# Optimization experiments

Hardware: AMD Instinct MI355X
Metric: run time of the kernel (lower is better)

The kernel has to match this reference:

```python
import jax, jax.numpy as jnp
import numpy as np

B, T, INPUT = 8, 16, 64
OUTPUT = 128
N_IN, N_TR, N_ACT = 32, 192, 32
N = N_IN + N_TR + N_ACT
H = 256   # neuron_hidden_dim
KQ = 256  # key_query_dim
S = 256   # signal_dim

def _xavier(key, shape):
    fan_in, fan_out = shape[-2], shape[-1]
    lim = np.sqrt(6.0 / (fan_in + fan_out)).astype(np.float32)
    return jax.random.uniform(key, shape, jnp.float32, -lim, lim)

def setup_inputs() -> dict:
    key = jax.random.key(0)
    ks = jax.random.split(key, 10)
    return {
        'x': jax.random.normal(ks[0], (B, T, INPUT), jnp.float32),
        'w_rec_input': _xavier(ks[1], (N_IN, INPUT, H)),
        'b_rec_input': jnp.zeros((N_IN, H), jnp.float32),
        'w_rec_other': _xavier(ks[2], (N_TR + N_ACT, S, H)),
        'b_rec_other': jnp.zeros((N_TR + N_ACT, H), jnp.float32),
        'w_lstm_ih': _xavier(ks[3], (N, H, 4 * H)),
        'b_lstm_ih': jnp.zeros((N, 4 * H), jnp.float32),
        'w_lstm_hh': _xavier(ks[4], (N, H, 4 * H)),
        'b_lstm_hh': jnp.zeros((N, 4 * H), jnp.float32),
        'w_query': _xavier(ks[5], (N, H, KQ)),
        'b_query': jnp.zeros((N, KQ), jnp.float32),
        'w_key': _xavier(ks[6], (N, H, KQ)),
        'b_key': jnp.zeros((N, KQ), jnp.float32),
        'w_sender': _xavier(ks[7], (N, H, S)),
        'b_sender': jnp.zeros((N, S), jnp.float32),
        'w_proj': _xavier(ks[8], (OUTPUT, N_ACT * S)),  # nn.Linear weight [out, in]
        'b_proj': jnp.zeros((OUTPUT,), jnp.float32),
    }

def reference(x, w_rec_input, b_rec_input, w_rec_other, b_rec_other,
              w_lstm_ih, b_lstm_ih, w_lstm_hh, b_lstm_hh,
              w_query, b_query, w_key, b_key, w_sender, b_sender,
              w_proj, b_proj):
    batch = x.shape[0]
    scale = 1.0 / np.sqrt(KQ).astype(np.float32)

    def step(carry, x_t):
        h, c, prev = carry  # [B,N,H], [B,N,H], [B,N,S]
        Q = jnp.einsum('bnh,nhk->bnk', h, w_query) + b_query
        K = jnp.einsum('bnh,nhk->bnk', h, w_key) + b_key
        scores = jnp.einsum('bnk,bmk->bnm', Q, K) * scale
        weights = jax.nn.softmax(scores, axis=2)
        ctx = jnp.einsum('bnm,bms->bns', weights, prev)  # [B,N,S]
        rec_in = jnp.einsum('bi,nih->bnh', x_t, w_rec_input) + b_rec_input  # [B,N_IN,H]
        rec_oth = jnp.einsum('bns,nsh->bnh', ctx[:, N_IN:, :], w_rec_other) + b_rec_other
        lstm_in = jax.nn.relu(jnp.concatenate([rec_in, rec_oth], axis=1))  # [B,N,H]
        gates = (jnp.einsum('bnh,nhg->bng', lstm_in, w_lstm_ih) + b_lstm_ih
                 + jnp.einsum('bnh,nhg->bng', h, w_lstm_hh) + b_lstm_hh)
        i_g, f_g, g_g, o_g = jnp.split(gates, 4, axis=2)
        c_new = jax.nn.sigmoid(f_g) * c + jax.nn.sigmoid(i_g) * jnp.tanh(g_g)
        h_new = jax.nn.sigmoid(o_g) * jnp.tanh(c_new)
        prev_new = jnp.einsum('bnh,nhs->bns', h_new, w_sender) + b_sender
        action = prev_new[:, -N_ACT:, :].reshape(batch, -1)
        out = action @ w_proj.T + b_proj
        return (h_new, c_new, prev_new), out

    init = (jnp.zeros((batch, N, H), x.dtype),
            jnp.zeros((batch, N, H), x.dtype),
            jnp.zeros((batch, N, S), x.dtype))
    _, outs = jax.lax.scan(step, init, jnp.swapaxes(x, 0, 1))  # outs: [T,B,OUTPUT]
    return jnp.swapaxes(outs, 0, 1)
```

## Files before the change

kernel.cpp:

```cpp
#include <hip/hip_runtime.h>
#include <cmath>

#define DEV_INLINE __device__ __forceinline__

constexpr int B_ = 8, T_ = 16, INPUT_ = 64, OUTPUT_ = 128;
constexpr int N_ = 256, H_ = 256, KQ_ = 256, S_ = 256, G_ = 1024;
constexpr int NIN_ = 32;
constexpr float SCALE_ = 0.0625f;

DEV_INLINE float sigmoid_(float x) { return 1.0f / (1.0f + expf(-x)); }
DEV_INLINE void fma4(float4& a, const float4& w, float s) {
    a.x += w.x * s; a.y += w.y * s; a.z += w.z * s; a.w += w.w * s;
}

__global__ __launch_bounds__(64)
void pnmm64_kernel(const float* __restrict__ in,
                   const float* __restrict__ W0, float* __restrict__ P0,
                   const float* __restrict__ W1, float* __restrict__ P1,
                   int n0)
{
    constexpr int KS = 4, HS = 256 / KS;
    const int ny = blockIdx.y;
    const int n = n0 + ny;
    const int split = blockIdx.x;
    const int lane = threadIdx.x;
    const int c0 = lane * 4;
    const int h0 = split * HS;
    const float* W = blockIdx.z ? W1 : W0;
    float* P = blockIdx.z ? P1 : P0;

    __shared__ float sh[HS * 8];
    for (int i = lane; i < HS * 8; i += 64) {
        int hh = i & (HS - 1), b = i >> 6;
        sh[hh * 8 + b] = in[(size_t)(b * N_ + n) * 256 + h0 + hh];
    }
    __syncthreads();

    const float* wp = W + ((size_t)ny * 256 + h0) * 256 + c0;
    float4 acc[8] = {};
    float4 bufA[8], bufB[8];
#pragma unroll
    for (int u = 0; u < 8; ++u) bufA[u] = *(const float4*)(wp + (size_t)u * 256);
#pragma unroll 1
    for (int hb = 0; hb < HS; hb += 8) {
        if (hb + 8 < HS) {
#pragma unroll
            for (int u = 0; u < 8; ++u)
                bufB[u] = *(const float4*)(wp + (size_t)(hb + 8 + u) * 256);
        }
#pragma unroll
        for (int u = 0; u < 8; ++u) {
            float4 w = bufA[u];
            const float* ip = &sh[(hb + u) * 8];
            float4 i0 = *(const float4*)ip;
            float4 i1 = *(const float4*)(ip + 4);
            fma4(acc[0], w, i0.x); fma4(acc[1], w, i0.y);
            fma4(acc[2], w, i0.z); fma4(acc[3], w, i0.w);
            fma4(acc[4], w, i1.x); fma4(acc[5], w, i1.y);
            fma4(acc[6], w, i1.z); fma4(acc[7], w, i1.w);
        }
#pragma unroll
        for (int u = 0; u < 8; ++u) bufA[u] = bufB[u];
    }
#pragma unroll
    for (int b = 0; b < 8; ++b)
        *(float4*)&P[(((size_t)split * 8 + b) * N_ + n) * 256 + c0] = acc[b];
}

__global__ __launch_bounds__(256)
void gates_mm_kernel(const float* __restrict__ lin, const float* __restrict__ hbuf,
                     const float* __restrict__ wih, const float* __restrict__ whh,
                     float* __restrict__ P)
{
    constexpr int KS = 2, HS = 256 / KS;
    const int n = blockIdx.y;
    const int split = blockIdx.x;
    const int tid = threadIdx.x;
    const int c0 = tid * 4;
    const int h0 = split * HS;

    __shared__ float shi[HS * 8];
    __shared__ float shh[HS * 8];
    for (int i = tid; i < HS * 8; i += 256) {
        int hh = i & (HS - 1), b = i >> 7;
        int src = (b * N_ + n) * H_ + h0 + hh;
        shi[hh * 8 + b] = lin[src];
        shh[hh * 8 + b] = hbuf[src];
    }
    __syncthreads();

    const float* wi = wih + ((size_t)n * H_ + h0) * G_ + c0;
    const float* wh = whh + ((size_t)n * H_ + h0) * G_ + c0;
    float4 acc[8] = {};
    float4 biA[4], bhA[4], biB[4], bhB[4];
#pragma unroll
    for (int u = 0; u < 4; ++u) {
        biA[u] = *(const float4*)(wi + (size_t)u * G_);
        bhA[u] = *(const float4*)(wh + (size_t)u * G_);
    }
#pragma unroll 1
    for (int hb = 0; hb < HS; hb += 4) {
        if (hb + 4 < HS) {
#pragma unroll
            for (int u = 0; u < 4; ++u) {
                biB[u] = *(const float4*)(wi + (size_t)(hb + 4 + u) * G_);
                bhB[u] = *(const float4*)(wh + (size_t)(hb + 4 + u) * G_);
            }
        }
#pragma unroll
        for (int u = 0; u < 4; ++u) {
            float4 a = biA[u];
            float4 h = bhA[u];
            const float* ip = &shi[(hb + u) * 8];
            const float* hp = &shh[(hb + u) * 8];
            float4 i0 = *(const float4*)ip;
            float4 i1 = *(const float4*)(ip + 4);
            float4 h0v = *(const float4*)hp;
            float4 h1v = *(const float4*)(hp + 4);
            fma4(acc[0], a, i0.x); fma4(acc[0], h, h0v.x);
            fma4(acc[1], a, i0.y); fma4(acc[1], h, h0v.y);
            fma4(acc[2], a, i0.z); fma4(acc[2], h, h0v.z);
            fma4(acc[3], a, i0.w); fma4(acc[3], h, h0v.w);
            fma4(acc[4], a, i1.x); fma4(acc[4], h, h1v.x);
            fma4(acc[5], a, i1.y); fma4(acc[5], h, h1v.y);
            fma4(acc[6], a, i1.z); fma4(acc[6], h, h1v.z);
            fma4(acc[7], a, i1.w); fma4(acc[7], h, h1v.w);
        }
#pragma unroll
        for (int u = 0; u < 4; ++u) { biA[u] = biB[u]; bhA[u] = bhB[u]; }
    }
#pragma unroll
    for (int b = 0; b < 8; ++b)
        *(float4*)&P[(((size_t)split * 8 + b) * N_ + n) * G_ + c0] = acc[b];
}

__global__ __launch_bounds__(256)
void rec_in_kernel(const float* __restrict__ x, int t,
                   const float* __restrict__ w_ri, const float* __restrict__ b_ri,
                   float* __restrict__ lin)
{
    __shared__ float sh[INPUT_ * 8];
    const int n = blockIdx.x;
    const int tid = threadIdx.x;
    for (int i = tid; i < INPUT_ * 8; i += 256) {
        int hh = i & 63, b = i >> 6;
        sh[hh * 8 + b] = x[((size_t)b * T_ + t) * INPUT_ + hh];
    }
    __syncthreads();
    const float* wp = w_ri + (size_t)n * INPUT_ * H_ + tid;
    float acc[8] = {};
#pragma unroll 8
    for (int hh = 0; hh < INPUT_; ++hh) {
        float w = wp[(size_t)hh * H_];
        float4 i0 = *(const float4*)&sh[hh * 8];
        float4 i1 = *(const float4*)&sh[hh * 8 + 4];
        acc[0] += w * i0.x; acc[1] += w * i0.y; acc[2] += w * i0.z; acc[3] += w * i0.w;
        acc[4] += w * i1.x; acc[5] += w * i1.y; acc[6] += w * i1.z; acc[7] += w * i1.w;
    }
    float bv = b_ri[n * H_ + tid];
#pragma unroll
    for (int b = 0; b < 8; ++b)
        lin[(size_t)(b * N_ + n) * H_ + tid] = fmaxf(acc[b] + bv, 0.f);
}

__global__ __launch_bounds__(256)
void reduce4_kernel(const float* __restrict__ P, const float* __restrict__ bias,
                    float* __restrict__ out, int n0, int nCount, int relu)
{
    const int idx = blockIdx.x * 256 + threadIdx.x;
    const int h4 = idx & 63;
    const int rest = idx >> 6;
    const int nn = rest % nCount;
    const int b = rest / nCount;
    const int n = n0 + nn;
    float4 s = *(const float4*)&bias[nn * 256 + h4 * 4];
#pragma unroll
    for (int sp = 0; sp < 4; ++sp) {
        float4 p = *(const float4*)&P[(((size_t)sp * 8 + b) * N_ + n) * 256 + h4 * 4];
        s.x += p.x; s.y += p.y; s.z += p.z; s.w += p.w;
    }
    if (relu) {
        s.x = fmaxf(s.x, 0.f); s.y = fmaxf(s.y, 0.f);
        s.z = fmaxf(s.z, 0.f); s.w = fmaxf(s.w, 0.f);
    }
    *(float4*)&out[((size_t)b * N_ + n) * 256 + h4 * 4] = s;
}

__global__ __launch_bounds__(256)
void reduceQK_kernel(const float* __restrict__ Pq, const float* __restrict__ Pk,
                     const float* __restrict__ bq, const float* __restrict__ bk,
                     float* __restrict__ Q, float* __restrict__ K)
{
    const int z = blockIdx.y;
    const float* P = z ? Pk : Pq;
    const float* bias = z ? bk : bq;
    float* out = z ? K : Q;
    const int idx = blockIdx.x * 256 + threadIdx.x;
    const int h4 = idx & 63;
    const int rest = idx >> 6;
    const int n = rest & 255;
    const int b = rest >> 8;
    float4 s = *(const float4*)&bias[n * 256 + h4 * 4];
#pragma unroll
    for (int sp = 0; sp < 4; ++sp) {
        float4 p = *(const float4*)&P[(((size_t)sp * 8 + b) * N_ + n) * 256 + h4 * 4];
        s.x += p.x; s.y += p.y; s.z += p.z; s.w += p.w;
    }
    *(float4*)&out[((size_t)b * N_ + n) * 256 + h4 * 4] = s;
}

__global__ void scores_kernel(const float* __restrict__ Q, const float* __restrict__ Kb,
                              float* __restrict__ sc)
{
    __shared__ float As[16][64];
    __shared__ float Bs[16][64];
    const int b = blockIdx.y;
    const int tile = blockIdx.x;
    const int row0 = (tile >> 2) * 64;
    const int col0 = (tile & 3) * 64;
    const int tid = threadIdx.x;
    const int tx = tid & 15, ty = tid >> 4;
    const int lr = tid >> 2;
    const int kq = (tid & 3) * 4;
    const float* Qb = Q + (size_t)b * N_ * KQ_;
    const float* Kbb = Kb + (size_t)b * N_ * KQ_;
    float acc[4][4] = {};
    for (int kt = 0; kt < KQ_; kt += 16) {
        float4 av = *(const float4*)&Qb[(size_t)(row0 + lr) * KQ_ + kt + kq];
        float4 bv = *(const float4*)&Kbb[(size_t)(col0 + lr) * KQ_ + kt + kq];
        __syncthreads();
        As[kq + 0][lr] = av.x; As[kq + 1][lr] = av.y; As[kq + 2][lr] = av.z; As[kq + 3][lr] = av.w;
        Bs[kq + 0][lr] = bv.x; Bs[kq + 1][lr] = bv.y; Bs[kq + 2][lr] = bv.z; Bs[kq + 3][lr] = bv.w;
        __syncthreads();
#pragma unroll
        for (int k = 0; k < 16; ++k) {
            float4 a = *(const float4*)&As[k][ty * 4];
            float4 c = *(const float4*)&Bs[k][tx * 4];
            acc[0][0] += a.x * c.x; acc[0][1] += a.x * c.y; acc[0][2] += a.x * c.z; acc[0][3] += a.x * c.w;
            acc[1][0] += a.y * c.x; acc[1][1] += a.y * c.y; acc[1][2] += a.y * c.z; acc[1][3] += a.y * c.w;
            acc[2][0] += a.z * c.x; acc[2][1] += a.z * c.y; acc[2][2] += a.z * c.z; acc[2][3] += a.z * c.w;
            acc[3][0] += a.w * c.x; acc[3][1] += a.w * c.y; acc[3][2] += a.w * c.z; acc[3][3] += a.w * c.w;
        }
    }
#pragma unroll
    for (int i = 0; i < 4; ++i) {
        float4 r = make_float4(acc[i][0] * SCALE_, acc[i][1] * SCALE_,
                               acc[i][2] * SCALE_, acc[i][3] * SCALE_);
        *(float4*)&sc[((size_t)b * N_ + row0 + ty * 4 + i) * N_ + col0 + tx * 4] = r;
    }
}

__global__ void softmax_kernel(float* __restrict__ sc)
{
    const int n = blockIdx.x, b = blockIdx.y;
    const int tid = threadIdx.x;
    __shared__ float red[256];
    float* row = sc + ((size_t)b * N_ + n) * N_;
    float v = row[tid];
    red[tid] = v;
    __syncthreads();
    for (int s = 128; s > 0; s >>= 1) {
        if (tid < s) red[tid] = fmaxf(red[tid], red[tid + s]);
        __syncthreads();
    }
    float m = red[0];
    __syncthreads();
    float e = expf(v - m);
    red[tid] = e;
    __syncthreads();
    for (int s = 128; s > 0; s >>= 1) {
        if (tid < s) red[tid] += red[tid + s];
        __syncthreads();
    }
    row[tid] = e / red[0];
}

__global__ void ctx_kernel(const float* __restrict__ W, const float* __restrict__ prev,
                           float* __restrict__ ctx)
{
    __shared__ float As[16][64];
    __shared__ float Bs[16][64];
    const int b = blockIdx.y;
    const int tile = blockIdx.x;
    const int row0 = (tile >> 2) * 64;
    const int col0 = (tile & 3) * 64;
    const int tid = threadIdx.x;
    const int tx = tid & 15, ty = tid >> 4;
    const int lr = tid >> 2;
    const int kq = (tid & 3) * 4;
    const int br = tid >> 4;
    const int bc = (tid & 15) * 4;
    const float* Wb = W + (size_t)b * N_ * N_;
    const float* pb = prev + (size_t)b * N_ * S_;
    float acc[4][4] = {};
    for (int kt = 0; kt < N_; kt += 16) {
        float4 av = *(const float4*)&Wb[(size_t)(row0 + lr) * N_ + kt + kq];
        float4 bv = *(const float4*)&pb[(size_t)(kt + br) * S_ + col0 + bc];
        __syncthreads();
        As[kq + 0][lr] = av.x; As[kq + 1][lr] = av.y; As[kq + 2][lr] = av.z; As[kq + 3][lr] = av.w;
        *(float4*)&Bs[br][bc] = bv;
        __syncthreads();
#pragma unroll
        for (int k = 0; k < 16; ++k) {
            float4 a = *(const float4*)&As[k][ty * 4];
            float4 c = *(const float4*)&Bs[k][tx * 4];
            acc[0][0] += a.x * c.x; acc[0][1] += a.x * c.y; acc[0][2] += a.x * c.z; acc[0][3] += a.x * c.w;
            acc[1][0] += a.y * c.x; acc[1][1] += a.y * c.y; acc[1][2] += a.y * c.z; acc[1][3] += a.y * c.w;
            acc[2][0] += a.z * c.x; acc[2][1] += a.z * c.y; acc[2][2] += a.z * c.z; acc[2][3] += a.z * c.w;
            acc[3][0] += a.w * c.x; acc[3][1] += a.w * c.y; acc[3][2] += a.w * c.z; acc[3][3] += a.w * c.w;
        }
    }
#pragma unroll
    for (int i = 0; i < 4; ++i) {
        float4 r = make_float4(acc[i][0], acc[i][1], acc[i][2], acc[i][3]);
        *(float4*)&ctx[((size_t)b * N_ + row0 + ty * 4 + i) * S_ + col0 + tx * 4] = r;
    }
}

__global__ __launch_bounds__(256)
void cell_kernel(const float* __restrict__ P, const float* __restrict__ bih,
                 const float* __restrict__ bhh,
                 float* __restrict__ c, float* __restrict__ h)
{
    const int tid = blockIdx.x * 256 + threadIdx.x;
    const int bn = tid >> 8;
    const int hx = tid & 255;
    const int n = bn & 255;
    const size_t PG = (size_t)8 * N_ * G_;
    const size_t gb = (size_t)bn * G_;
    float g4[4];
#pragma unroll
    for (int gi = 0; gi < 4; ++gi) {
        int off = gi * 256 + hx;
        g4[gi] = P[gb + off] + P[PG + gb + off]
               + bih[n * G_ + off] + bhh[n * G_ + off];
    }
    float cv = c[tid];
    float cn = sigmoid_(g4[1]) * cv + sigmoid_(g4[0]) * tanhf(g4[2]);
    float hn = sigmoid_(g4[3]) * tanhf(cn);
    c[tid] = cn;
    h[tid] = hn;
}

__global__ void proj_kernel(const float* __restrict__ prev, const float* __restrict__ wp,
                            const float* __restrict__ bp, float* __restrict__ out, int t)
{
    const int o = blockIdx.x;
    const int tid = threadIdx.x;
    float acc[8] = {};
    const float* wr = wp + (size_t)o * (32 * S_);
    for (int j = tid; j < 32 * S_; j += 256) {
        float w = wr[j];
#pragma unroll
        for (int b = 0; b < 8; ++b)
            acc[b] += w * prev[(size_t)b * N_ * S_ + 224 * S_ + j];
    }
    __shared__ float red[256];
#pragma unroll
    for (int b = 0; b < 8; ++b) {
        red[tid] = acc[b];
        __syncthreads();
        for (int s = 128; s > 0; s >>= 1) {
            if (tid < s) red[tid] += red[tid + s];
            __syncthreads();
        }
        if (tid == 0) out[((size_t)b * T_ + t) * OUTPUT_ + o] = red[0] + bp[o];
        __syncthreads();
    }
}

extern "C" void kernel_launch(void* const* d_in, const int* in_sizes, int n_in,
                              void* d_out, int out_size, void* d_ws, size_t ws_size,
                              hipStream_t stream)
{
    (void)in_sizes; (void)n_in; (void)out_size; (void)ws_size;
    const float* x    = (const float*)d_in[0];
    const float* w_ri = (const float*)d_in[1];
    const float* b_ri = (const float*)d_in[2];
    const float* w_ro = (const float*)d_in[3];
    const float* b_ro = (const float*)d_in[4];
    const float* w_ih = (const float*)d_in[5];
    const float* b_ih = (const float*)d_in[6];
    const float* w_hh = (const float*)d_in[7];
    const float* b_hh = (const float*)d_in[8];
    const float* w_q  = (const float*)d_in[9];
    const float* b_q  = (const float*)d_in[10];
    const float* w_k  = (const float*)d_in[11];
    const float* b_k  = (const float*)d_in[12];
    const float* w_s  = (const float*)d_in[13];
    const float* b_s  = (const float*)d_in[14];
    const float* w_p  = (const float*)d_in[15];
    const float* b_p  = (const float*)d_in[16];
    float* out = (float*)d_out;

    float* ws = (float*)d_ws;
    const size_t SZ = (size_t)B_ * N_ * H_;
    float* hbuf = ws;
    float* cbuf = hbuf + SZ;
    float* prev = cbuf + SZ;
    float* Q    = prev + SZ;
    float* Kb   = Q + SZ;
    float* sc   = Kb + SZ;
    float* ctxb = sc + SZ;
    float* lin  = ctxb + SZ;
    float* Pbuf = lin + SZ;
    float* Pq   = Pbuf;
    float* Pk   = Pbuf + 4 * SZ;
    float* Prec = Pbuf;
    float* Pg   = Pbuf;
    float* Ps   = Pbuf;

    hipMemsetAsync(d_ws, 0, 3 * SZ * sizeof(float), stream);

    for (int t = 0; t < T_; ++t) {
        pnmm64_kernel<<<dim3(4, 256, 2), 64, 0, stream>>>(hbuf, w_q, Pq, w_k, Pk, 0);
        reduceQK_kernel<<<dim3(512, 2), 256, 0, stream>>>(Pq, Pk, b_q, b_k, Q, Kb);
        scores_kernel<<<dim3(16, B_), 256, 0, stream>>>(Q, Kb, sc);
        softmax_kernel<<<dim3(N_, B_), 256, 0, stream>>>(sc);
        ctx_kernel<<<dim3(16, B_), 256, 0, stream>>>(sc, prev, ctxb);
        rec_in_kernel<<<dim3(NIN_), 256, 0, stream>>>(x, t, w_ri, b_ri, lin);
        pnmm64_kernel<<<dim3(4, 224, 1), 64, 0, stream>>>(ctxb, w_ro, Prec, w_ro, Prec, NIN_);
        reduce4_kernel<<<dim3(448), 256, 0, stream>>>(Prec, b_ro, lin, NIN_, 224, 1);
        gates_mm_kernel<<<dim3(2, 256), 256, 0, stream>>>(lin, hbuf, w_ih, w_hh, Pg);
        cell_kernel<<<dim3(2048), 256, 0, stream>>>(Pg, b_ih, b_hh, cbuf, hbuf);
        pnmm64_kernel<<<dim3(4, 256, 1), 64, 0, stream>>>(hbuf, w_s, Ps, w_s, Ps, 0);
        reduce4_kernel<<<dim3(512), 256, 0, stream>>>(Ps, b_s, prev, 0, 256, 0);
        proj_kernel<<<dim3(OUTPUT_), 256, 0, stream>>>(prev, w_p, b_p, out, t);
    }
}
```

Measured before the change: 4.483 ms.

## Fuse split-K reductions, softmax+ctx, gates+cell, and hoist input recurrence

Replaces the split-K matmul kernels plus separate reduce kernels with in-block LDS reductions that apply bias and relu directly. Merges softmax into the context matmul, gates matmul into the LSTM cell update, and computes sender/Q/K projections in one launch at the end of each step. The input-neuron recurrence is precomputed for all timesteps up front, and the projection kernel uses wave shuffles. Together these cut kernel launches and the global traffic for partial sums, at the cost of fewer, larger blocks and possibly lower occupancy.

Measured after the change: 3.922 ms. 1.14x faster.

```diff
diff --git a/kernel.cpp b/kernel.cpp
--- a/kernel.cpp
+++ b/kernel.cpp
@@ -13,37 +13,44 @@
     a.x += w.x * s; a.y += w.y * s; a.z += w.z * s; a.w += w.w * s;
 }
 
-__global__ __launch_bounds__(64)
-void pnmm64_kernel(const float* __restrict__ in,
-                   const float* __restrict__ W0, float* __restrict__ P0,
-                   const float* __restrict__ W1, float* __restrict__ P1,
-                   int n0)
-{
-    constexpr int KS = 4, HS = 256 / KS;
-    const int ny = blockIdx.y;
+__global__ __launch_bounds__(256)
+void pnmm256_kernel(const float* __restrict__ in,
+                    const float* __restrict__ W0, const float* __restrict__ bias0, float* __restrict__ O0,
+                    const float* __restrict__ W1, const float* __restrict__ bias1, float* __restrict__ O1,
+                    const float* __restrict__ W2, const float* __restrict__ bias2, float* __restrict__ O2,
+                    int n0, int nW0, int relu)
+{
+    const int ny = blockIdx.x;
     const int n = n0 + ny;
-    const int split = blockIdx.x;
-    const int lane = threadIdx.x;
+    const int nw = n - nW0;
+    const float* W; const float* bias; float* O;
+    if (blockIdx.y == 0)      { W = W0; bias = bias0; O = O0; }
+    else if (blockIdx.y == 1) { W = W1; bias = bias1; O = O1; }
+    else                      { W = W2; bias = bias2; O = O2; }
+
+    const int tid = threadIdx.x;
+    const int wv = tid >> 6;
+    const int lane = tid & 63;
     const int c0 = lane * 4;
-    const int h0 = split * HS;
-    const float* W = blockIdx.z ? W1 : W0;
-    float* P = blockIdx.z ? P1 : P0;
-
-    __shared__ float sh[HS * 8];
-    for (int i = lane; i < HS * 8; i += 64) {
-        int hh = i & (HS - 1), b = i >> 6;
-        sh[hh * 8 + b] = in[(size_t)(b * N_ + n) * 256 + h0 + hh];
-    }
-    __syncthreads();
-
-    const float* wp = W + ((size_t)ny * 256 + h0) * 256 + c0;
+    const int h0 = wv * 64;
+
+    __shared__ float sh[256 * 8];
+    __shared__ float psum[4][2048];
+
+    for (int i = tid; i < 2048; i += 256) {
+        int hh = i & 255, b = i >> 8;
+        sh[hh * 8 + b] = in[(size_t)(b * N_ + n) * H_ + hh];
+    }
+    __syncthreads();
+
+    const float* wp = W + ((size_t)nw * H_ + h0) * 256 + c0;
     float4 acc[8] = {};
     float4 bufA[8], bufB[8];
 #pragma unroll
     for (int u = 0; u < 8; ++u) bufA[u] = *(const float4*)(wp + (size_t)u * 256);
 #pragma unroll 1
-    for (int hb = 0; hb < HS; hb += 8) {
-        if (hb + 8 < HS) {
+    for (int hb = 0; hb < 64; hb += 8) {
+        if (hb + 8 < 64) {
 #pragma unroll
             for (int u = 0; u < 8; ++u)
                 bufB[u] = *(const float4*)(wp + (size_t)(hb + 8 + u) * 256);
@@ -51,7 +58,7 @@
 #pragma unroll
         for (int u = 0; u < 8; ++u) {
             float4 w = bufA[u];
-            const float* ip = &sh[(hb + u) * 8];
+            const float* ip = &sh[(h0 + hb + u) * 8];
             float4 i0 = *(const float4*)ip;
             float4 i1 = *(const float4*)(ip + 4);
             fma4(acc[0], w, i0.x); fma4(acc[1], w, i0.y);
@@ -64,28 +71,43 @@
     }
 #pragma unroll
     for (int b = 0; b < 8; ++b)
-        *(float4*)&P[(((size_t)split * 8 + b) * N_ + n) * 256 + c0] = acc[b];
-}
-
-__global__ __launch_bounds__(256)
-void gates_mm_kernel(const float* __restrict__ lin, const float* __restrict__ hbuf,
-                     const float* __restrict__ wih, const float* __restrict__ whh,
-                     float* __restrict__ P)
-{
-    constexpr int KS = 2, HS = 256 / KS;
-    const int n = blockIdx.y;
-    const int split = blockIdx.x;
+        *(float4*)&psum[wv][b * 256 + c0] = acc[b];
+    __syncthreads();
+
+    for (int i = tid; i < 2048; i += 256) {
+        int b = i >> 8, cc = i & 255;
+        float s = psum[0][i] + psum[1][i] + psum[2][i] + psum[3][i]
+                + bias[(size_t)nw * 256 + cc];
+        if (relu) s = fmaxf(s, 0.f);
+        O[(size_t)(b * N_ + n) * H_ + cc] = s;
+    }
+}
+
+__global__ __launch_bounds__(512)
+void gatescell_kernel(const float* __restrict__ lin,
+                      const float* __restrict__ rec_all,
+                      int t,
+                      const float* __restrict__ wih, const float* __restrict__ whh,
+                      const float* __restrict__ bih, const float* __restrict__ bhh,
+                      float* __restrict__ c, float* __restrict__ h)
+{
+    const int n = blockIdx.x;
     const int tid = threadIdx.x;
-    const int c0 = tid * 4;
-    const int h0 = split * HS;
-
-    __shared__ float shi[HS * 8];
-    __shared__ float shh[HS * 8];
-    for (int i = tid; i < HS * 8; i += 256) {
-        int hh = i & (HS - 1), b = i >> 7;
-        int src = (b * N_ + n) * H_ + h0 + hh;
-        shi[hh * 8 + b] = lin[src];
-        shh[hh * 8 + b] = hbuf[src];
+    const int sp = tid >> 8;
+    const int c0 = (tid & 255) * 4;
+    const int h0 = sp * 128;
+
+    __shared__ float smem[8192];
+    float* shi = smem;
+    float* shh = smem + 2048;
+    float* glds = smem;
+
+    for (int i = tid; i < 2048; i += 512) {
+        int hh = i & 255, b = i >> 8;
+        shh[hh * 8 + b] = h[(size_t)(b * N_ + n) * H_ + hh];
+        shi[hh * 8 + b] = (n < NIN_)
+            ? rec_all[(((size_t)t * 8 + b) * NIN_ + n) * H_ + hh]
+            : lin[(size_t)(b * N_ + n) * H_ + hh];
     }
     __syncthreads();
 
@@ -99,8 +121,8 @@
         bhA[u] = *(const float4*)(wh + (size_t)u * G_);
     }
 #pragma unroll 1
-    for (int hb = 0; hb < HS; hb += 4) {
-        if (hb + 4 < HS) {
+    for (int hb = 0; hb < 128; hb += 4) {
+        if (hb + 4 < 128) {
 #pragma unroll
             for (int u = 0; u < 4; ++u) {
                 biB[u] = *(const float4*)(wi + (size_t)(hb + 4 + u) * G_);
@@ -110,37 +132,70 @@
 #pragma unroll
         for (int u = 0; u < 4; ++u) {
             float4 a = biA[u];
-            float4 h = bhA[u];
-            const float* ip = &shi[(hb + u) * 8];
-            const float* hp = &shh[(hb + u) * 8];
+            float4 hv = bhA[u];
+            const float* ip = &shi[(h0 + hb + u) * 8];
+            const float* hp = &shh[(h0 + hb + u) * 8];
             float4 i0 = *(const float4*)ip;
             float4 i1 = *(const float4*)(ip + 4);
             float4 h0v = *(const float4*)hp;
             float4 h1v = *(const float4*)(hp + 4);
-            fma4(acc[0], a, i0.x); fma4(acc[0], h, h0v.x);
-            fma4(acc[1], a, i0.y); fma4(acc[1], h, h0v.y);
-            fma4(acc[2], a, i0.z); fma4(acc[2], h, h0v.z);
-            fma4(acc[3], a, i0.w); fma4(acc[3], h, h0v.w);
-            fma4(acc[4], a, i1.x); fma4(acc[4], h, h1v.x);
-            fma4(acc[5], a, i1.y); fma4(acc[5], h, h1v.y);
-            fma4(acc[6], a, i1.z); fma4(acc[6], h, h1v.z);
-            fma4(acc[7], a, i1.w); fma4(acc[7], h, h1v.w);
+            fma4(acc[0], a, i0.x); fma4(acc[0], hv, h0v.x);
+            fma4(acc[1], a, i0.y); fma4(acc[1], hv, h0v.y);
+            fma4(acc[2], a, i0.z); fma4(acc[2], hv, h0v.z);
+            fma4(acc[3], a, i0.w); fma4(acc[3], hv, h0v.w);
+            fma4(acc[4], a, i1.x); fma4(acc[4], hv, h1v.x);
+            fma4(acc[5], a, i1.y); fma4(acc[5], hv, h1v.y);
+            fma4(acc[6], a, i1.z); fma4(acc[6], hv, h1v.z);
+            fma4(acc[7], a, i1.w); fma4(acc[7], hv, h1v.w);
         }
 #pragma unroll
         for (int u = 0; u < 4; ++u) { biA[u] = biB[u]; bhA[u] = bhB[u]; }
     }
-#pragma unroll
-    for (int b = 0; b < 8; ++b)
-        *(float4*)&P[(((size_t)split * 8 + b) * N_ + n) * G_ + c0] = acc[b];
+    __syncthreads();
+    if (sp == 1) {
+#pragma unroll
+        for (int b = 0; b < 8; ++b)
+            *(float4*)&glds[b * 1024 + c0] = acc[b];
+    }
+    __syncthreads();
+    if (sp == 0) {
+        float4 bi = *(const float4*)&bih[(size_t)n * G_ + c0];
+        float4 bh = *(const float4*)&bhh[(size_t)n * G_ + c0];
+#pragma unroll
+        for (int b = 0; b < 8; ++b) {
+            float4 g = *(const float4*)&glds[b * 1024 + c0];
+            g.x += acc[b].x + bi.x + bh.x;
+            g.y += acc[b].y + bi.y + bh.y;
+            g.z += acc[b].z + bi.z + bh.z;
+            g.w += acc[b].w + bi.w + bh.w;
+            *(float4*)&glds[b * 1024 + c0] = g;
+        }
+    }
+    __syncthreads();
+#pragma unroll
+    for (int e = 0; e < 4; ++e) {
+        int idx = tid + 512 * e;
+        int b = idx >> 8, hx = idx & 255;
+        float ig = glds[b * 1024 + 0   + hx];
+        float fg = glds[b * 1024 + 256 + hx];
+        float gg = glds[b * 1024 + 512 + hx];
+        float og = glds[b * 1024 + 768 + hx];
+        size_t off = (size_t)(b * N_ + n) * H_ + hx;
+        float cv = c[off];
+        float cn = sigmoid_(fg) * cv + sigmoid_(ig) * tanhf(gg);
+        c[off] = cn;
+        h[off] = sigmoid_(og) * tanhf(cn);
+    }
 }
 
 __global__ __launch_bounds__(256)
-void rec_in_kernel(const float* __restrict__ x, int t,
-                   const float* __restrict__ w_ri, const float* __restrict__ b_ri,
-                   float* __restrict__ lin)
+void rec_in_all_kernel(const float* __restrict__ x,
+                       const float* __restrict__ w_ri, const float* __restrict__ b_ri,
+                       float* __restrict__ rec_all)
 {
     __shared__ float sh[INPUT_ * 8];
     const int n = blockIdx.x;
+    const int t = blockIdx.y;
     const int tid = threadIdx.x;
     for (int i = tid; i < INPUT_ * 8; i += 256) {
         int hh = i & 63, b = i >> 6;
@@ -160,53 +215,7 @@
     float bv = b_ri[n * H_ + tid];
 #pragma unroll
     for (int b = 0; b < 8; ++b)
-        lin[(size_t)(b * N_ + n) * H_ + tid] = fmaxf(acc[b] + bv, 0.f);
-}
-
-__global__ __launch_bounds__(256)
-void reduce4_kernel(const float* __restrict__ P, const float* __restrict__ bias,
-                    float* __restrict__ out, int n0, int nCount, int relu)
-{
-    const int idx = blockIdx.x * 256 + threadIdx.x;
-    const int h4 = idx & 63;
-    const int rest = idx >> 6;
-    const int nn = rest % nCount;
-    const int b = rest / nCount;
-    const int n = n0 + nn;
-    float4 s = *(const float4*)&bias[nn * 256 + h4 * 4];
-#pragma unroll
-    for (int sp = 0; sp < 4; ++sp) {
-        float4 p = *(const float4*)&P[(((size_t)sp * 8 + b) * N_ + n) * 256 + h4 * 4];
-        s.x += p.x; s.y += p.y; s.z += p.z; s.w += p.w;
-    }
-    if (relu) {
-        s.x = fmaxf(s.x, 0.f); s.y = fmaxf(s.y, 0.f);
-        s.z = fmaxf(s.z, 0.f); s.w = fmaxf(s.w, 0.f);
-    }
-    *(float4*)&out[((size_t)b * N_ + n) * 256 + h4 * 4] = s;
-}
-
-__global__ __launch_bounds__(256)
-void reduceQK_kernel(const float* __restrict__ Pq, const float* __restrict__ Pk,
-                     const float* __restrict__ bq, const float* __restrict__ bk,
-                     float* __restrict__ Q, float* __restrict__ K)
-{
-    const int z = blockIdx.y;
-    const float* P = z ? Pk : Pq;
-    const float* bias = z ? bk : bq;
-    float* out = z ? K : Q;
-    const int idx = blockIdx.x * 256 + threadIdx.x;
-    const int h4 = idx & 63;
-    const int rest = idx >> 6;
-    const int n = rest & 255;
-    const int b = rest >> 8;
-    float4 s = *(const float4*)&bias[n * 256 + h4 * 4];
-#pragma unroll
-    for (int sp = 0; sp < 4; ++sp) {
-        float4 p = *(const float4*)&P[(((size_t)sp * 8 + b) * N_ + n) * 256 + h4 * 4];
-        s.x += p.x; s.y += p.y; s.z += p.z; s.w += p.w;
-    }
-    *(float4*)&out[((size_t)b * N_ + n) * 256 + h4 * 4] = s;
+        rec_all[(((size_t)t * 8 + b) * NIN_ + n) * H_ + tid] = fmaxf(acc[b] + bv, 0.f);
 }
 
 __global__ void scores_kernel(const float* __restrict__ Q, const float* __restrict__ Kb,
@@ -250,59 +259,68 @@
     }
 }
 
-__global__ void softmax_kernel(float* __restrict__ sc)
-{
-    const int n = blockIdx.x, b = blockIdx.y;
-    const int tid = threadIdx.x;
-    __shared__ float red[256];
-    float* row = sc + ((size_t)b * N_ + n) * N_;
-    float v = row[tid];
-    red[tid] = v;
-    __syncthreads();
-    for (int s = 128; s > 0; s >>= 1) {
-        if (tid < s) red[tid] = fmaxf(red[tid], red[tid + s]);
-        __syncthreads();
-    }
-    float m = red[0];
-    __syncthreads();
-    float e = expf(v - m);
-    red[tid] = e;
-    __syncthreads();
-    for (int s = 128; s > 0; s >>= 1) {
-        if (tid < s) red[tid] += red[tid + s];
-        __syncthreads();
-    }
-    row[tid] = e / red[0];
-}
-
-__global__ void ctx_kernel(const float* __restrict__ W, const float* __restrict__ prev,
-                           float* __restrict__ ctx)
-{
-    __shared__ float As[16][64];
+__global__ __launch_bounds__(256)
+void smctx_kernel(const float* __restrict__ sc, const float* __restrict__ prev,
+                  float* __restrict__ ctx)
+{
+    __shared__ float Ws[256][68];
     __shared__ float Bs[16][64];
+    __shared__ float redm[4][64];
+    __shared__ float reds[4][64];
+    __shared__ float rmax[64];
+    __shared__ float rinv[64];
+
     const int b = blockIdx.y;
     const int tile = blockIdx.x;
     const int row0 = (tile >> 2) * 64;
     const int col0 = (tile & 3) * 64;
     const int tid = threadIdx.x;
+    const int r = tid & 63;
+    const int q = tid >> 6;
+
+    const float* srow = sc + ((size_t)b * N_ + row0 + r) * N_ + q * 64;
+    float lmax = -3.4e38f;
+#pragma unroll
+    for (int i = 0; i < 16; ++i) {
+        float4 v = *(const float4*)&srow[4 * i];
+        Ws[q * 64 + 4 * i + 0][r] = v.x;
+        Ws[q * 64 + 4 * i + 1][r] = v.y;
+        Ws[q * 64 + 4 * i + 2][r] = v.z;
+        Ws[q * 64 + 4 * i + 3][r] = v.w;
+        lmax = fmaxf(lmax, fmaxf(fmaxf(v.x, v.y), fmaxf(v.z, v.w)));
+    }
+    redm[q][r] = lmax;
+    __syncthreads();
+    if (tid < 64)
+        rmax[tid] = fmaxf(fmaxf(redm[0][tid], redm[1][tid]),
+                          fmaxf(redm[2][tid], redm[3][tid]));
+    __syncthreads();
+    {
+        float m = rmax[r];
+        float lsum = 0.f;
+#pragma unroll 4
+        for (int i = 0; i < 64; ++i) {
+            float e = expf(Ws[q * 64 + i][r] - m);
+            Ws[q * 64 + i][r] = e;
+            lsum += e;
+        }
+        reds[q][r] = lsum;
+    }
+    __syncthreads();
+    if (tid < 64)
+        rinv[tid] = 1.0f / (reds[0][tid] + reds[1][tid] + reds[2][tid] + reds[3][tid]);
+
     const int tx = tid & 15, ty = tid >> 4;
-    const int lr = tid >> 2;
-    const int kq = (tid & 3) * 4;
-    const int br = tid >> 4;
-    const int bc = (tid & 15) * 4;
-    const float* Wb = W + (size_t)b * N_ * N_;
-    const float* pb = prev + (size_t)b * N_ * S_;
+    const int br = tid >> 4, bc = (tid & 15) * 4;
     float acc[4][4] = {};
     for (int kt = 0; kt < N_; kt += 16) {
-        float4 av = *(const float4*)&Wb[(size_t)(row0 + lr) * N_ + kt + kq];
-        float4 bv = *(const float4*)&pb[(size_t)(kt + br) * S_ + col0 + bc];
+        float4 bv = *(const float4*)&prev[((size_t)b * N_ + kt + br) * S_ + col0 + bc];
         __syncthreads();
-        As[kq + 0][lr] = av.x; As[kq + 1][lr] = av.y; As[kq + 2][lr] = av.z; As[kq + 3][lr] = av.w;
         *(float4*)&Bs[br][bc] = bv;
         __syncthreads();
 #pragma unroll
         for (int k = 0; k < 16; ++k) {
-            float4 a = *(const float4*)&As[k][ty * 4];
+            float4 a = *(const float4*)&Ws[kt + k][ty * 4];
             float4 c = *(const float4*)&Bs[k][tx * 4];
             acc[0][0] += a.x * c.x; acc[0][1] += a.x * c.y; acc[0][2] += a.x * c.z; acc[0][3] += a.x * c.w;
             acc[1][0] += a.y * c.x; acc[1][1] += a.y * c.y; acc[1][2] += a.y * c.z; acc[1][3] += a.y * c.w;
@@ -312,60 +330,38 @@
     }
 #pragma unroll
     for (int i = 0; i < 4; ++i) {
-        float4 r = make_float4(acc[i][0], acc[i][1], acc[i][2], acc[i][3]);
-        *(float4*)&ctx[((size_t)b * N_ + row0 + ty * 4 + i) * S_ + col0 + tx * 4] = r;
-    }
-}
-
-__global__ __launch_bounds__(256)
-void cell_kernel(const float* __restrict__ P, const float* __restrict__ bih,
-                 const float* __restrict__ bhh,
-                 float* __restrict__ c, float* __restrict__ h)
-{
-    const int tid = blockIdx.x * 256 + threadIdx.x;
-    const int bn = tid >> 8;
-    const int hx = tid & 255;
-    const int n = bn & 255;
-    const size_t PG = (size_t)8 * N_ * G_;
-    const size_t gb = (size_t)bn * G_;
-    float g4[4];
-#pragma unroll
-    for (int gi = 0; gi < 4; ++gi) {
-        int off = gi * 256 + hx;
-        g4[gi] = P[gb + off] + P[PG + gb + off]
-               + bih[n * G_ + off] + bhh[n * G_ + off];
-    }
-    float cv = c[tid];
-    float cn = sigmoid_(g4[1]) * cv + sigmoid_(g4[0]) * tanhf(g4[2]);
-    float hn = sigmoid_(g4[3]) * tanhf(cn);
-    c[tid] = cn;
-    h[tid] = hn;
-}
-
-__global__ void proj_kernel(const float* __restrict__ prev, const float* __restrict__ wp,
-                            const float* __restrict__ bp, float* __restrict__ out, int t)
+        float inv = rinv[ty * 4 + i];
+        float4 rr = make_float4(acc[i][0] * inv, acc[i][1] * inv,
+                                acc[i][2] * inv, acc[i][3] * inv);
+        *(float4*)&ctx[((size_t)b * N_ + row0 + ty * 4 + i) * S_ + col0 + tx * 4] = rr;
+    }
+}
+
+__global__ __launch_bounds__(64)
+void proj64_kernel(const float* __restrict__ prev, const float* __restrict__ wp,
+                   const float* __restrict__ bp, float* __restrict__ out, int t)
 {
     const int o = blockIdx.x;
-    const int tid = threadIdx.x;
+    const int lane = threadIdx.x;
+    const float* wr = wp + (size_t)o * (NIN_ * S_);
     float acc[8] = {};
-    const float* wr = wp + (size_t)o * (32 * S_);
-    for (int j = tid; j < 32 * S_; j += 256) {
-        float w = wr[j];
+    for (int i = lane * 4; i < NIN_ * S_; i += 256) {
+        float4 w = *(const float4*)&wr[i];
+#pragma unroll
+        for (int b = 0; b < 8; ++b) {
+            float4 p = *(const float4*)&prev[((size_t)b * N_ + (N_ - NIN_)) * S_ + i];
+            acc[b] += w.x * p.x + w.y * p.y + w.z * p.z + w.w * p.w;
+        }
+    }
+#pragma unroll
+    for (int b = 0; b < 8; ++b)
+        for (int off = 32; off > 0; off >>= 1)
+            acc[b] += __shfl_down(acc[b], off);
+    if (lane == 0) {
+        float bv = bp[o];
 #pragma unroll
         for (int b = 0; b < 8; ++b)
-            acc[b] += w * prev[(size_t)b * N_ * S_ + 224 * S_ + j];
-    }
-    __shared__ float red[256];
-#pragma unroll
-    for (int b = 0; b < 8; ++b) {
-        red[tid] = acc[b];
-        __syncthreads();
-        for (int s = 128; s > 0; s >>= 1) {
-            if (tid < s) red[tid] += red[tid + s];
-            __syncthreads();
-        }
-        if (tid == 0) out[((size_t)b * T_ + t) * OUTPUT_ + o] = red[0] + bp[o];
-        __syncthreads();
+            out[((size_t)b * T_ + t) * OUTPUT_ + o] = acc[b] + bv;
     }
 }
 
@@ -403,28 +399,23 @@
     float* sc   = Kb + SZ;
     float* ctxb = sc + SZ;
     float* lin  = ctxb + SZ;
-    float* Pbuf = lin + SZ;
-    float* Pq   = Pbuf;
-    float* Pk   = Pbuf + 4 * SZ;
-    float* Prec = Pbuf;
-    float* Pg   = Pbuf;
-    float* Ps   = Pbuf;
+    float* rec_all = lin + SZ;
 
     hipMemsetAsync(d_ws, 0, 3 * SZ * sizeof(float), stream);
 
+    rec_in_all_kernel<<<dim3(NIN_, T_), 256, 0, stream>>>(x, w_ri, b_ri, rec_all);
+    pnmm256_kernel<<<dim3(256, 2), 256, 0, stream>>>(hbuf,
+        w_q, b_q, Q, w_k, b_k, Kb, w_k, b_k, Kb, 0, 0, 0);
+
     for (int t = 0; t < T_; ++t) {
-        pnmm64_kernel<<<dim3(4, 256, 2), 64, 0, stream>>>(hbuf, w_q, Pq, w_k, Pk, 0);
-        reduceQK_kernel<<<dim3(512, 2), 256, 0, stream>>>(Pq, Pk, b_q, b_k, Q, Kb);
         scores_kernel<<<dim3(16, B_), 256, 0, stream>>>(Q, Kb, sc);
-        softmax_kernel<<<dim3(N_, B_), 256, 0, stream>>>(sc);
-        ctx_kernel<<<dim3(16, B_), 256, 0, stream>>>(sc, prev, ctxb);
-        rec_in_kernel<<<dim3(NIN_), 256, 0, stream>>>(x, t, w_ri, b_ri, lin);
-        pnmm64_kernel<<<dim3(4, 224, 1), 64, 0, stream>>>(ctxb, w_ro, Prec, w_ro, Prec, NIN_);
-        reduce4_kernel<<<dim3(448), 256, 0, stream>>>(Prec, b_ro, lin, NIN_, 224, 1);
-        gates_mm_kernel<<<dim3(2, 256), 256, 0, stream>>>(lin, hbuf, w_ih, w_hh, Pg);
-        cell_kernel<<<dim3(2048), 256, 0, stream>>>(Pg, b_ih, b_hh, cbuf, hbuf);
-        pnmm64_kernel<<<dim3(4, 256, 1), 64, 0, stream>>>(hbuf, w_s, Ps, w_s, Ps, 0);
-        reduce4_kernel<<<dim3(512), 256, 0, stream>>>(Ps, b_s, prev, 0, 256, 0);
-        proj_kernel<<<dim3(OUTPUT_), 256, 0, stream>>>(prev, w_p, b_p, out, t);
-    }
-}
+        smctx_kernel<<<dim3(16, B_), 256, 0, stream>>>(sc, prev, ctxb);
+        pnmm256_kernel<<<dim3(224, 1), 256, 0, stream>>>(ctxb,
+            w_ro, b_ro, lin, w_ro, b_ro, lin, w_ro, b_ro, lin, NIN_, NIN_, 1);
+        gatescell_kernel<<<dim3(256), 512, 0, stream>>>(lin, rec_all, t,
+            w_ih, w_hh, b_ih, b_hh, cbuf, hbuf);
+        pnmm256_kernel<<<dim3(256, 3), 256, 0, stream>>>(hbuf,
+            w_s, b_s, prev, w_q, b_q, Q, w_k, b_k, Kb, 0, 0, 0);
+        proj64_kernel<<<dim3(OUTPUT_), 64, 0, stream>>>(prev, w_p, b_p, out, t);
+    }
+}
```
